# Performance work log

Measured on AMD Instinct MI355X. Metric: run time of the kernel, lower is better.

## Reference

```python
import jax, jax.numpy as jnp
import numpy as np

B, S, C = 8, 2048, 512

def setup_inputs() -> dict:
    key = jax.random.key(0)
    ks = jax.random.split(key, 7)
    s = 1.0 / np.sqrt(C)
    return {
        "x": jax.random.normal(ks[0], (B, S, C), dtype=jnp.float32),
        "Wq": jax.random.uniform(ks[1], (C, C), jnp.float32, -s, s),
        "bq": jax.random.uniform(ks[2], (C,), jnp.float32, -s, s),
        "Wk": jax.random.uniform(ks[3], (C, C), jnp.float32, -s, s),
        "bk": jax.random.uniform(ks[4], (C,), jnp.float32, -s, s),
        "Wv": jax.random.uniform(ks[5], (C, C), jnp.float32, -s, s),
        "bv": jax.random.uniform(ks[6], (C,), jnp.float32, -s, s),
    }

def reference(x, Wq, bq, Wk, bk, Wv, bv):
    # Linear projections (torch Linear: x @ W.T + b)
    q = jnp.einsum('bsc,dc->bsd', x, Wq) + bq
    k = jnp.einsum('bsc,dc->bsd', x, Wk) + bk
    v = jnp.einsum('bsc,dc->bsd', x, Wv) + bv
    # NOTE: original code computes dk but never scales by 1/sqrt(dk)
    scores = jnp.einsum('bqd,bkd->bqk', q, k)          # [B,S,S]
    attn = jax.nn.softmax(scores, axis=-1)
    out = jnp.einsum('bqk,bkd->bqd', attn, v)
    return out + x
```

## Files before the change

### kernel.cpp

```cpp
#include <hip/hip_runtime.h>
#include <hip/hip_bf16.h>


typedef __bf16 bf16_t;
typedef bf16_t bf16x8 __attribute__((ext_vector_type(8)));
typedef float floatx4 __attribute__((ext_vector_type(4)));

#define MFMA16(a, b, c) __builtin_amdgcn_mfma_f32_16x16x32_bf16((a), (b), (c), 0, 0, 0)
#define FLASH_LDS 136704

__device__ __forceinline__ void gload16(const void* g, void* l) {
    __builtin_amdgcn_global_load_lds((const __attribute__((address_space(1))) void*)g,
                                     (__attribute__((address_space(3))) void*)l, 16, 0, 0);
}

__device__ __forceinline__ float wave16_sum(float v) {
    v += __shfl_xor(v, 1);
    v += __shfl_xor(v, 2);
    v += __shfl_xor(v, 4);
    v += __shfl_xor(v, 8);
    return v;
}

__global__ void convert_in(const float* __restrict__ X,
                           const float* __restrict__ Wq, const float* __restrict__ Wk,
                           const float* __restrict__ Wv, const float* __restrict__ bq,
                           const float* __restrict__ bk, const float* __restrict__ bv,
                           bf16_t* __restrict__ Xb, bf16_t* __restrict__ Wb,
                           float* __restrict__ biasc) {
    int bid = blockIdx.x, tid = threadIdx.x;
    if (bid < 4096) {
        size_t e0 = ((size_t)bid * 256 + tid) * 8;
        float4 f0 = *(const float4*)(X + e0);
        float4 f1 = *(const float4*)(X + e0 + 4);
        bf16x8 o;
        o[0] = (bf16_t)f0.x; o[1] = (bf16_t)f0.y; o[2] = (bf16_t)f0.z; o[3] = (bf16_t)f0.w;
        o[4] = (bf16_t)f1.x; o[5] = (bf16_t)f1.y; o[6] = (bf16_t)f1.z; o[7] = (bf16_t)f1.w;
        *(bf16x8*)(Xb + e0) = o;
    } else {
        int idx = (bid - 4096) * 256 + tid;
        int e0 = idx * 4;
        int row = e0 >> 9, c = e0 & 511;
        const float* src;
        if (row < 512)       src = Wq + row * 512;
        else if (row < 1024) src = Wk + (row - 512) * 512;
        else                 src = Wv + (row - 1024) * 512;
        float4 v = *(const float4*)(src + c);
        bf16_t w4[4] = {(bf16_t)v.x, (bf16_t)v.y, (bf16_t)v.z, (bf16_t)v.w};
        *(int2*)(Wb + e0) = *(const int2*)w4;
        if (idx < 1536) {
            float b;
            if (idx < 512)       b = bq[idx];
            else if (idx < 1024) b = bk[idx - 512];
            else                 b = bv[idx - 1024];
            biasc[idx] = b;
        }
    }
}

__global__ __launch_bounds__(256, 2)
void qkv_gemm(const bf16_t* __restrict__ Xb, const bf16_t* __restrict__ Wb,
              const float* __restrict__ biasc, bf16_t* __restrict__ Q,
              bf16_t* __restrict__ K, bf16_t* __restrict__ Vt) {
    __shared__ int4 smem4[4096];
    char* base = (char*)smem4;
    char* Tile = (char*)smem4;

    const int tid = threadIdx.x;
    const int l = tid & 63, w = tid >> 6;
    const int lane16 = l & 15, lq = l >> 4;
    const int klo = lane16 & 7;
    const int m0 = (blockIdx.x & 127) << 7;
    const int n0 = (blockIdx.x >> 7) << 7;
    const int wm = (w >> 1) << 6, wn = (w & 1) << 6;
    const int srow = l >> 3;
    const int sc8 = (l & 7) ^ srow;

    auto stage = [&](int it, int buf) {
        char* As = base + buf * 32768;
        char* Bs = As + 16384;
#pragma unroll
        for (int j = 0; j < 4; ++j) {
            int seg = j * 4 + w;
            int row = seg * 8 + srow;
            gload16(Xb + (size_t)(m0 + row) * 512 + it * 64 + sc8 * 8, As + seg * 1024);
            gload16(Wb + (size_t)(n0 + row) * 512 + it * 64 + sc8 * 8, Bs + seg * 1024);
        }
    };

    floatx4 acc[4][4];
#pragma unroll
    for (int a = 0; a < 4; ++a)
#pragma unroll
        for (int bb = 0; bb < 4; ++bb) acc[a][bb] = (floatx4){0.f, 0.f, 0.f, 0.f};

    stage(0, 0);
    __syncthreads();

    for (int it = 0; it < 8; ++it) {
        if (it < 7) stage(it + 1, (it + 1) & 1);
        char* As = base + (it & 1) * 32768;
        char* Bs = As + 16384;
#pragma unroll
        for (int kst = 0; kst < 2; ++kst) {
            bf16x8 afr[4], bfr[4];
#pragma unroll
            for (int mt = 0; mt < 4; ++mt)
                afr[mt] = *(const bf16x8*)(As + (wm + mt * 16 + lane16) * 128 +
                                           ((kst * 4 + lq) ^ klo) * 16);
#pragma unroll
            for (int nt = 0; nt < 4; ++nt)
                bfr[nt] = *(const bf16x8*)(Bs + (wn + nt * 16 + lane16) * 128 +
                                           ((kst * 4 + lq) ^ klo) * 16);
#pragma unroll
            for (int mt = 0; mt < 4; ++mt)
#pragma unroll
                for (int nt = 0; nt < 4; ++nt)
                    acc[mt][nt] = MFMA16(afr[mt], bfr[nt], acc[mt][nt]);
        }
        __syncthreads();
    }

    float bias_v[4];
#pragma unroll
    for (int nt = 0; nt < 4; ++nt) bias_v[nt] = biasc[n0 + wn + nt * 16 + lane16];

    if (n0 < 1024) {
        bf16_t* Dst = (n0 < 512) ? Q : K;
        const int coff0 = (n0 < 512) ? n0 : n0 - 512;
#pragma unroll
        for (int mt = 0; mt < 4; ++mt)
#pragma unroll
            for (int nt = 0; nt < 4; ++nt)
#pragma unroll
                for (int i = 0; i < 4; ++i) {
                    int sl = wm + mt * 16 + lq * 4 + i;
                    int dl = wn + nt * 16 + lane16;
                    *(bf16_t*)(Tile + sl * 264 + dl * 2) =
                        (bf16_t)(acc[mt][nt][i] + bias_v[nt]);
                }
        __syncthreads();
#pragma unroll
        for (int j = 0; j < 8; ++j) {
            int slot = j * 256 + tid;
            int row = slot >> 4, c = slot & 15;
            *(int4*)(Dst + (size_t)(m0 + row) * 512 + coff0 + c * 8) =
                *(const int4*)(Tile + row * 264 + c * 16);
        }
    } else {
#pragma unroll
        for (int mt = 0; mt < 4; ++mt)
#pragma unroll
            for (int nt = 0; nt < 4; ++nt)
#pragma unroll
                for (int i = 0; i < 4; ++i) {
                    int dl = wn + nt * 16 + lane16;
                    int sl = wm + mt * 16 + lq * 4 + i;
                    *(bf16_t*)(Tile + dl * 264 + sl * 2) =
                        (bf16_t)(acc[mt][nt][i] + bias_v[nt]);
                }
        __syncthreads();
        const int bb = m0 >> 11, s0 = m0 & 2047, dbase = n0 - 1024;
#pragma unroll
        for (int j = 0; j < 8; ++j) {
            int slot = j * 256 + tid;
            int dd = slot >> 4, c = slot & 15;
            *(int4*)(Vt + (size_t)(bb * 512 + dbase + dd) * 2048 + s0 + c * 8) =
                *(const int4*)(Tile + dd * 264 + c * 16);
        }
    }
}

__global__ __launch_bounds__(512, 2)
void flash_attn_v7(const bf16_t* __restrict__ Q, const bf16_t* __restrict__ K,
                   const bf16_t* __restrict__ Vt, const float* __restrict__ X,
                   float* __restrict__ Out) {
    extern __shared__ char smem[];
    char* Ps = smem + 131072;
    float* lpart = (float*)(smem + 136192);

    const int tid = threadIdx.x;
    const int l = tid & 63, w = tid >> 6;
    const int lane16 = l & 15, lq = l >> 4;
    const int qg = w >> 1, h = w & 1;
    const int dbase = w << 6;
    const int b = blockIdx.x & 7;
    const int q0 = (blockIdx.x >> 3) << 6;

    const bf16_t* Kbase = K + (size_t)b * 2048 * 512;
    const bf16_t* Vbase = Vt + (size_t)b * 512 * 2048;

    const int dl_v = ((l >> 3) << 1) | ((l & 7) >> 2);
    const int vc   = (l & 3) ^ ((l >> 3) & 3);

    auto stageK = [&](int kt, char* Kb) {
#pragma unroll
        for (int j = 0; j < 4; ++j) {
            int seg = j * 8 + w;
            int c = (l & ~7) | ((l & 7) ^ (seg & 7));
            gload16(Kbase + ((size_t)kt * 32 + seg) * 512 + c * 8, Kb + seg * 1024);
        }
    };
    auto stageV = [&](int kt, char* Vb) {
        const bf16_t* Vsrc = Vbase + kt * 32;
#pragma unroll
        for (int j = 0; j < 4; ++j) {
            int seg = j * 8 + w;
            int d = seg * 16 + dl_v;
            gload16(Vsrc + (size_t)d * 2048 + vc * 8, Vb + seg * 1024);
        }
    };

    stageK(0, smem);
    stageV(0, smem + 65536);

    bf16x8 qf[16];
    const bf16_t* Qrow = Q + (size_t)(b * 2048 + q0 + qg * 16 + lane16) * 512 + lq * 8;
#pragma unroll
    for (int kst = 0; kst < 16; ++kst) qf[kst] = *(const bf16x8*)(Qrow + kst * 32);

    floatx4 o[16];
#pragma unroll
    for (int t = 0; t < 16; ++t) o[t] = (floatx4){0.f, 0.f, 0.f, 0.f};
    float lsum[4] = {0.f, 0.f, 0.f, 0.f};
    const float L2E = 1.4426950408889634f;
    const int key = h * 16 + lane16;

    __syncthreads();

    for (int kt = 0; kt < 64; ++kt) {
        char* Kcur = smem + (kt & 1) * 32768;
        char* Vcur = smem + 65536 + (kt & 1) * 32768;

        if (kt < 63) {
            stageK(kt + 1, smem + ((kt + 1) & 1) * 32768);
            stageV(kt + 1, smem + 65536 + ((kt + 1) & 1) * 32768);
        }

        floatx4 sc = (floatx4){0.f, 0.f, 0.f, 0.f};
#pragma unroll
        for (int kst = 0; kst < 16; ++kst) {
            int i0 = kst * 4 + lq;
            int p0 = (i0 & ~7) | ((i0 & 7) ^ (key & 7));
            bf16x8 kb = *(const bf16x8*)(Kcur + key * 1024 + p0 * 16);
            sc = MFMA16(qf[kst], kb, sc);
        }

#pragma unroll
        for (int i = 0; i < 4; ++i) {
            int row = qg * 16 + lq * 4 + i;
            float p = __builtin_exp2f(sc[i] * L2E);
            lsum[i] += p;
            *(bf16_t*)(Ps + row * 80 + key * 2) = (bf16_t)p;
        }

        asm volatile("s_waitcnt lgkmcnt(0)\n\ts_barrier" ::: "memory");
        __builtin_amdgcn_sched_barrier(0);

        bf16x8 pa[4], vb[4];
#pragma unroll
        for (int qgi = 0; qgi < 4; ++qgi)
            pa[qgi] = *(const bf16x8*)(Ps + (qgi * 16 + lane16) * 80 + lq * 16);
#pragma unroll
        for (int dg = 0; dg < 4; ++dg) {
            int d = dbase + dg * 16 + lane16;
            int slot = (d & 1) * 4 + (lq ^ ((d >> 1) & 3));
            vb[dg] = *(const bf16x8*)(Vcur + (d >> 1) * 128 + slot * 16);
        }
#pragma unroll
        for (int dg = 0; dg < 4; ++dg)
#pragma unroll
            for (int qgi = 0; qgi < 4; ++qgi)
                o[qgi * 4 + dg] = MFMA16(pa[qgi], vb[dg], o[qgi * 4 + dg]);

        __syncthreads();
    }

#pragma unroll
    for (int i = 0; i < 4; ++i) {
        float s = wave16_sum(lsum[i]);
        if (lane16 == 0) lpart[(qg * 16 + lq * 4 + i) * 2 + h] = s;
    }
    __syncthreads();

#pragma unroll
    for (int qgi = 0; qgi < 4; ++qgi) {
        float rinv[4];
#pragma unroll
        for (int i = 0; i < 4; ++i) {
            int row = qgi * 16 + lq * 4 + i;
            rinv[i] = 1.0f / (lpart[row * 2] + lpart[row * 2 + 1]);
        }
#pragma unroll
        for (int dg = 0; dg < 4; ++dg) {
            int d = dbase + dg * 16 + lane16;
#pragma unroll
            for (int i = 0; i < 4; ++i) {
                int row = q0 + qgi * 16 + lq * 4 + i;
                size_t g = (size_t)(b * 2048 + row) * 512 + d;
                Out[g] = o[qgi * 4 + dg][i] * rinv[i] + X[g];
            }
        }
    }
}

extern "C" void kernel_launch(void* const* d_in, const int* in_sizes, int n_in,
                              void* d_out, int out_size, void* d_ws, size_t ws_size,
                              hipStream_t stream) {
    const float* x  = (const float*)d_in[0];
    const float* Wq = (const float*)d_in[1];
    const float* bq = (const float*)d_in[2];
    const float* Wk = (const float*)d_in[3];
    const float* bk = (const float*)d_in[4];
    const float* Wv = (const float*)d_in[5];
    const float* bv = (const float*)d_in[6];
    float* out = (float*)d_out;
    char* ws = (char*)d_ws;

    bf16_t* Wb    = (bf16_t*)(ws);
    float*  biasc = (float*)(ws + 1572864);
    bf16_t* Xb    = (bf16_t*)(ws + 1579008);
    bf16_t* Qb    = (bf16_t*)(ws + 18356224);
    bf16_t* Kb    = (bf16_t*)(ws + 35133440);
    bf16_t* Vt    = (bf16_t*)(ws + 51910656);

    convert_in<<<4864, 256, 0, stream>>>(x, Wq, Wk, Wv, bq, bk, bv, Xb, Wb, biasc);
    qkv_gemm<<<1536, 256, 0, stream>>>(Xb, Wb, biasc, Qb, Kb, Vt);

    hipFuncSetAttribute(reinterpret_cast<const void*>(flash_attn_v7),
                        hipFuncAttributeMaxDynamicSharedMemorySize, FLASH_LDS);
    flash_attn_v7<<<256, 512, FLASH_LDS, stream>>>(Qb, Kb, Vt, x, out);
}
```

Before: 224.0 us.

## Enlarge QKV GEMM tile to 256x128 with 512 threads and fragment-native LDS layout

The QKV projection GEMM now uses 256x128 output tiles per block with 8 waves (768 blocks instead of 1536). The K step per stage shrinks to 32, and LDS holds data in MFMA fragment order, so each lane reads its fragment with one contiguous 16-byte load and no XOR swizzle. The aim is more reuse of each weight tile and cheaper fragment addressing, in exchange for twice as many K iterations and barriers, larger dynamic LDS, and fewer blocks to spread across CUs. Epilogue tile strides and store loops are adjusted for the taller tile.

Result: slower. 239.7 us (+7.0%).

```diff
diff --git a/kernel.cpp b/kernel.cpp
--- a/kernel.cpp
+++ b/kernel.cpp
@@ -8,6 +8,7 @@
 
 #define MFMA16(a, b, c) __builtin_amdgcn_mfma_f32_16x16x32_bf16((a), (b), (c), 0, 0, 0)
 #define FLASH_LDS 136704
+#define QKV_LDS 67584
 
 __device__ __forceinline__ void gload16(const void* g, void* l) {
     __builtin_amdgcn_global_load_lds((const __attribute__((address_space(1))) void*)g,
@@ -58,33 +59,35 @@
     }
 }
 
-__global__ __launch_bounds__(256, 2)
+__global__ __launch_bounds__(512, 2)
 void qkv_gemm(const bf16_t* __restrict__ Xb, const bf16_t* __restrict__ Wb,
               const float* __restrict__ biasc, bf16_t* __restrict__ Q,
               bf16_t* __restrict__ K, bf16_t* __restrict__ Vt) {
-    __shared__ int4 smem4[4096];
-    char* base = (char*)smem4;
-    char* Tile = (char*)smem4;
+    extern __shared__ char base[];
+    char* Tile = base;
 
     const int tid = threadIdx.x;
     const int l = tid & 63, w = tid >> 6;
     const int lane16 = l & 15, lq = l >> 4;
-    const int klo = lane16 & 7;
-    const int m0 = (blockIdx.x & 127) << 7;
-    const int n0 = (blockIdx.x >> 7) << 7;
+    const int m0 = (blockIdx.x & 63) << 8;
+    const int n0 = (blockIdx.x >> 6) << 7;
     const int wm = (w >> 1) << 6, wn = (w & 1) << 6;
-    const int srow = l >> 3;
-    const int sc8 = (l & 7) ^ srow;
 
     auto stage = [&](int it, int buf) {
-        char* As = base + buf * 32768;
+        char* As = base + buf * 24576;
         char* Bs = As + 16384;
 #pragma unroll
-        for (int j = 0; j < 4; ++j) {
-            int seg = j * 4 + w;
-            int row = seg * 8 + srow;
-            gload16(Xb + (size_t)(m0 + row) * 512 + it * 64 + sc8 * 8, As + seg * 1024);
-            gload16(Wb + (size_t)(n0 + row) * 512 + it * 64 + sc8 * 8, Bs + seg * 1024);
+        for (int j = 0; j < 3; ++j) {
+            int seg = j * 8 + w;
+            if (seg < 16) {
+                int row = seg * 16 + lane16;
+                gload16(Xb + (size_t)(m0 + row) * 512 + it * 32 + lq * 8,
+                        As + seg * 1024);
+            } else {
+                int row = (seg - 16) * 16 + lane16;
+                gload16(Wb + (size_t)(n0 + row) * 512 + it * 32 + lq * 8,
+                        Bs + (seg - 16) * 1024);
+            }
         }
     };
 
@@ -97,27 +100,22 @@
     stage(0, 0);
     __syncthreads();
 
-    for (int it = 0; it < 8; ++it) {
-        if (it < 7) stage(it + 1, (it + 1) & 1);
-        char* As = base + (it & 1) * 32768;
+    for (int it = 0; it < 16; ++it) {
+        if (it < 15) stage(it + 1, (it + 1) & 1);
+        char* As = base + (it & 1) * 24576;
         char* Bs = As + 16384;
-#pragma unroll
-        for (int kst = 0; kst < 2; ++kst) {
-            bf16x8 afr[4], bfr[4];
-#pragma unroll
-            for (int mt = 0; mt < 4; ++mt)
-                afr[mt] = *(const bf16x8*)(As + (wm + mt * 16 + lane16) * 128 +
-                                           ((kst * 4 + lq) ^ klo) * 16);
+        bf16x8 afr[4], bfr[4];
+#pragma unroll
+        for (int mt = 0; mt < 4; ++mt)
+            afr[mt] = *(const bf16x8*)(As + ((wm >> 4) + mt) * 1024 + l * 16);
+#pragma unroll
+        for (int nt = 0; nt < 4; ++nt)
+            bfr[nt] = *(const bf16x8*)(Bs + ((wn >> 4) + nt) * 1024 + l * 16);
+#pragma unroll
+        for (int mt = 0; mt < 4; ++mt)
 #pragma unroll
             for (int nt = 0; nt < 4; ++nt)
-                bfr[nt] = *(const bf16x8*)(Bs + (wn + nt * 16 + lane16) * 128 +
-                                           ((kst * 4 + lq) ^ klo) * 16);
-#pragma unroll
-            for (int mt = 0; mt < 4; ++mt)
-#pragma unroll
-                for (int nt = 0; nt < 4; ++nt)
-                    acc[mt][nt] = MFMA16(afr[mt], bfr[nt], acc[mt][nt]);
-        }
+                acc[mt][nt] = MFMA16(afr[mt], bfr[nt], acc[mt][nt]);
         __syncthreads();
     }
 
@@ -142,7 +140,7 @@
         __syncthreads();
 #pragma unroll
         for (int j = 0; j < 8; ++j) {
-            int slot = j * 256 + tid;
+            int slot = j * 512 + tid;
             int row = slot >> 4, c = slot & 15;
             *(int4*)(Dst + (size_t)(m0 + row) * 512 + coff0 + c * 8) =
                 *(const int4*)(Tile + row * 264 + c * 16);
@@ -156,17 +154,17 @@
                 for (int i = 0; i < 4; ++i) {
                     int dl = wn + nt * 16 + lane16;
                     int sl = wm + mt * 16 + lq * 4 + i;
-                    *(bf16_t*)(Tile + dl * 264 + sl * 2) =
+                    *(bf16_t*)(Tile + dl * 520 + sl * 2) =
                         (bf16_t)(acc[mt][nt][i] + bias_v[nt]);
                 }
         __syncthreads();
         const int bb = m0 >> 11, s0 = m0 & 2047, dbase = n0 - 1024;
 #pragma unroll
         for (int j = 0; j < 8; ++j) {
-            int slot = j * 256 + tid;
-            int dd = slot >> 4, c = slot & 15;
+            int slot = j * 512 + tid;
+            int dd = slot >> 5, c = slot & 31;
             *(int4*)(Vt + (size_t)(bb * 512 + dbase + dd) * 2048 + s0 + c * 8) =
-                *(const int4*)(Tile + dd * 264 + c * 16);
+                *(const int4*)(Tile + dd * 520 + c * 16);
         }
     }
 }
@@ -325,7 +323,10 @@
     bf16_t* Vt    = (bf16_t*)(ws + 51910656);
 
     convert_in<<<4864, 256, 0, stream>>>(x, Wq, Wk, Wv, bq, bk, bv, Xb, Wb, biasc);
-    qkv_gemm<<<1536, 256, 0, stream>>>(Xb, Wb, biasc, Qb, Kb, Vt);
+
+    hipFuncSetAttribute(reinterpret_cast<const void*>(qkv_gemm),
+                        hipFuncAttributeMaxDynamicSharedMemorySize, QKV_LDS);
+    qkv_gemm<<<768, 512, QKV_LDS, stream>>>(Xb, Wb, biasc, Qb, Kb, Vt);
 
     hipFuncSetAttribute(reinterpret_cast<const void*>(flash_attn_v7),
                         hipFuncAttributeMaxDynamicSharedMemorySize, FLASH_LDS);
```
